# Optimization experiments

Hardware: AMD Instinct MI355X
Metric: run time of the kernel (lower is better)

The kernel has to match this reference:

```python
import math
import jax
import jax.numpy as jnp
import numpy as np

MUL = 32            # multiplicity of 0e and 1o in irreps_in/out
N_NODES = 50000
N_EDGES = 800000
N_BASIS = 10
N_HID = 100
NUM_NEIGHBORS = 16.0


def setup_inputs() -> dict:
    key = jax.random.key(0)
    ks = jax.random.split(key, 14)
    return {
        "node_input": jax.random.normal(ks[0], (N_NODES, 4 * MUL), jnp.float32),
        "node_attr": jnp.ones((N_NODES, 1), jnp.float32),
        "edge_src": jax.random.randint(ks[1], (N_EDGES,), 0, N_NODES, dtype=jnp.int32),
        "edge_dst": jax.random.randint(ks[2], (N_EDGES,), 0, N_NODES, dtype=jnp.int32),
        "edge_attr": jax.random.normal(ks[3], (N_EDGES, 4), jnp.float32),
        "edge_length_embedded": jax.random.uniform(ks[4], (N_EDGES, N_BASIS), dtype=jnp.float32),
        "W_sc0": jax.random.normal(ks[5], (MUL, MUL), jnp.float32),
        "W_sc1": jax.random.normal(ks[6], (MUL, MUL), jnp.float32),
        "W_l10": jax.random.normal(ks[7], (MUL, MUL), jnp.float32),
        "W_l11": jax.random.normal(ks[8], (MUL, MUL), jnp.float32),
        "W_l20": jax.random.normal(ks[9], (2 * MUL, MUL), jnp.float32),
        "W_l21": jax.random.normal(ks[10], (2 * MUL, MUL), jnp.float32),
        "W_fc1": jax.random.normal(ks[11], (N_BASIS, N_HID), jnp.float32),
        "W_fc2": jax.random.normal(ks[12], (N_HID, 4 * MUL), jnp.float32),
    }


def _fctp(x0, x1, attr, W0, W1):
    """FullyConnectedTensorProduct with a 1x0e attr: per-irrep linear * scalar attr.
    x0: [N,U], x1: [N,U,3], attr: [N,1]. Path norm alpha = 1/sqrt(fan_in)."""
    inv = 1.0 / math.sqrt(W0.shape[0])
    o0 = attr * (x0 @ W0) * inv                                    # [N,W]
    o1 = attr[:, :, None] * jnp.einsum("nud,uw->nwd", x1, W1) * inv  # [N,W,3]
    return o0, o1


def _forward(node_input, node_attr, edge_attr, edge_length_embedded,
             W_sc0, W_sc1, W_l10, W_l11, W_l20, W_l21, W_fc1, W_fc2,
             edge_src, edge_dst):
    N = node_input.shape[0]
    x0 = node_input[:, :MUL]                       # [N,32]  0e
    x1 = node_input[:, MUL:].reshape(N, MUL, 3)    # [N,32,3] 1o

    # self-connection and lin1 (both attr is scalar 0e)
    s0, s1 = _fctp(x0, x1, node_attr, W_sc0, W_sc1)
    y0, y1 = _fctp(x0, x1, node_attr, W_l10, W_l11)

    # radial MLP -> per-edge uvu weights (weight_numel = 4*MUL)
    h = jax.nn.silu(edge_length_embedded @ W_fc1 * (1.0 / math.sqrt(N_BASIS)))
    w = h @ W_fc2 * (1.0 / math.sqrt(N_HID))       # [E,128]
    w1, w2, w3, w4 = (w[:, 0*MUL:1*MUL], w[:, 1*MUL:2*MUL],
                      w[:, 2*MUL:3*MUL], w[:, 3*MUL:4*MUL])

    # gather source node features per edge
    x0s = y0[edge_src]                              # [E,32]
    x1s = y1[edge_src]                              # [E,32,3]
    ea0 = edge_attr[:, :1]                          # [E,1]   0e
    ea1 = edge_attr[:, 1:]                          # [E,3]   1o

    # segmented uvu tensor product (CG for lmax=1, component norm)
    mid0a = w1 * x0s * ea0                                         # 0e x 0e -> 0e
    mid0b = w4 * jnp.einsum("eum,em->eu", x1s, ea1) * (1.0 / math.sqrt(3.0))  # 1o x 1o -> 0e
    mid1a = (w2 * x0s)[:, :, None] * ea1[:, None, :]               # 0e x 1o -> 1o
    mid1b = w3[:, :, None] * x1s * ea0[:, None, :]                 # 1o x 0e -> 1o
    E = edge_attr.shape[0]
    edge_features = jnp.concatenate(
        [mid0a, mid0b, mid1a.reshape(E, -1), mid1b.reshape(E, -1)], axis=1)  # [E,256]

    # scatter-add to destination nodes
    agg = jax.ops.segment_sum(edge_features, edge_dst, num_segments=N)
    agg = agg * (1.0 / math.sqrt(NUM_NEIGHBORS))

    m0 = agg[:, :2 * MUL]                           # [N,64]  0e part of irreps_mid
    m1 = agg[:, 2 * MUL:].reshape(N, 2 * MUL, 3)    # [N,64,3] 1o part
    z0, z1 = _fctp(m0, m1, node_attr, W_l20, W_l21)

    # sc output_mask is all ones (every output irrep reachable)
    c_s = math.sin(math.pi / 8.0)
    c_x = math.cos(math.pi / 8.0)
    out0 = c_s * s0 + c_x * z0
    out1 = c_s * s1 + c_x * z1
    return jnp.concatenate([out0, out1.reshape(N, -1)], axis=1)   # [N,128]


def reference(node_input, node_attr, edge_src, edge_dst, edge_attr, edge_length_embedded,
              W_sc0, W_sc1, W_l10, W_l11, W_l20, W_l21, W_fc1, W_fc2):
    return _forward(node_input, node_attr, edge_attr, edge_length_embedded,
                    W_sc0, W_sc1, W_l10, W_l11, W_l20, W_l21, W_fc1, W_fc2,
                    edge_src, edge_dst)
```

## Files before the change

### kernel.cpp

```cpp
#include <hip/hip_runtime.h>
#include <hip/hip_bf16.h>

#define MUL 32
#define F4 128
#define NB 10
#define NH 100
#define EROW 136
#define REC 48

#define INV_SQRT32 0.17677669529663687f
#define INV_SQRT10 0.31622776601683794f
#define INV_SQRT100 0.1f
#define INV_SQRT3 0.5773502691896258f
#define AGG_SCALE 0.25f
#define INV8 0.125f
#define C_S 0.3826834323650898f
#define C_X 0.9238795325112867f

typedef __attribute__((ext_vector_type(8))) short short8;
typedef __attribute__((ext_vector_type(4))) float float4v;

__device__ __forceinline__ float bf2f(__hip_bfloat16 v) { return __bfloat162float(v); }
__device__ __forceinline__ unsigned short f2b(float x) {
    __hip_bfloat16 b = __float2bfloat16(x);
    return *(unsigned short*)&b;
}
__device__ __forceinline__ float b2f(unsigned short u) {
    __hip_bfloat16 b;
    *(unsigned short*)&b = u;
    return __bfloat162float(b);
}
__device__ __forceinline__ float ldin(const void* p, size_t i, int f) {
    return f ? ((const float*)p)[i] : bf2f(((const __hip_bfloat16*)p)[i]);
}

__global__ void detect_dtype_kernel(const void* __restrict__ node_attr, int* __restrict__ flag) {
    unsigned w = *(const unsigned*)node_attr;
    *flag = (w == 0x3F800000u) ? 1 : 0;
}

__global__ __launch_bounds__(256) void prep_kernel(
    const void* __restrict__ Wfc1,
    const void* __restrict__ Wfc2,
    const void* __restrict__ Wl20,
    const void* __restrict__ Wl21,
    const int* __restrict__ flagp,
    unsigned short* __restrict__ w1t,
    unsigned short* __restrict__ w2t,
    unsigned short* __restrict__ w20t,
    unsigned short* __restrict__ w21t)
{
    int f = *flagp;
    int gi = blockIdx.x * 256 + threadIdx.x;
    if (gi < 128 * 128) {
        int n = gi >> 7, k = gi & 127;
        w2t[gi] = (k < NH) ? f2b(ldin(Wfc2, (size_t)k * 128 + n, f)) : 0;
    }
    if (gi < 32 * 64) {
        int v = gi >> 6, u = gi & 63;
        w20t[gi] = f2b(ldin(Wl20, (size_t)u * 32 + v, f));
        w21t[gi] = f2b(ldin(Wl21, (size_t)u * 32 + v, f));
    }
    if (gi < 112 * 32) {
        int n = gi >> 5, k = gi & 31;
        w1t[gi] = (k < NB && n < NH) ? f2b(ldin(Wfc1, (size_t)k * NH + n, f)) : 0;
    }
}

__global__ __launch_bounds__(256) void hist_kernel(
    const int* __restrict__ edst, int* __restrict__ cnt, int E)
{
    int i = blockIdx.x * 256 + threadIdx.x;
    if (i < E) atomicAdd(&cnt[edst[i]], 1);
}

__global__ __launch_bounds__(1024) void scanA_kernel(
    int* __restrict__ cnt, int* __restrict__ bsum, int N)
{
    __shared__ int wsum[16];
    int t = threadIdx.x, lane = t & 63, wid = t >> 6;
    int i = blockIdx.x * 1024 + t;
    int v = (i < N) ? cnt[i] : 0;
    int x = v;
#pragma unroll
    for (int d = 1; d < 64; d <<= 1) { int yv = __shfl_up(x, d); if (lane >= d) x += yv; }
    if (lane == 63) wsum[wid] = x;
    __syncthreads();
    if (wid == 0 && lane < 16) {
        int s = wsum[lane];
#pragma unroll
        for (int d = 1; d < 16; d <<= 1) { int yv = __shfl_up(s, d); if (lane >= d) s += yv; }
        wsum[lane] = s;
    }
    __syncthreads();
    int pre = (wid > 0 ? wsum[wid - 1] : 0);
    if (i < N) cnt[i] = pre + x - v;
    if (t == 0) bsum[blockIdx.x] = wsum[15];
}

__global__ __launch_bounds__(64) void scanB_kernel(int* __restrict__ bsum, int nb)
{
    int t = threadIdx.x;
    int carry = 0;
    for (int c0 = 0; c0 < nb; c0 += 64) {
        int idx = c0 + t;
        int v = (idx < nb) ? bsum[idx] : 0;
        int x = v;
#pragma unroll
        for (int d = 1; d < 64; d <<= 1) { int yv = __shfl_up(x, d); if (t >= d) x += yv; }
        if (idx < nb) bsum[idx] = carry + x - v;
        carry += __shfl(x, 63);
    }
}

__global__ __launch_bounds__(1024) void scanC_kernel(
    int* __restrict__ cnt, const int* __restrict__ bsum, int N)
{
    int i = blockIdx.x * 1024 + threadIdx.x;
    if (i < N) cnt[i] += bsum[blockIdx.x];
}

__global__ __launch_bounds__(256) void scatter_build_kernel(
    const int* __restrict__ edst,
    const int* __restrict__ esrc,
    const void* __restrict__ eattr,
    const void* __restrict__ ele,
    const int* __restrict__ flagp,
    int* __restrict__ cnt,
    unsigned char* __restrict__ rec, int E)
{
    int i = blockIdx.x * 256 + threadIdx.x;
    if (i >= E) return;
    int f = *flagp;
    int d = edst[i];
    int p = atomicAdd(&cnt[d], 1);

    unsigned e0 = f2b(ldin(ele, (size_t)i * NB + 0, f));
    unsigned e1 = f2b(ldin(ele, (size_t)i * NB + 1, f));
    unsigned e2 = f2b(ldin(ele, (size_t)i * NB + 2, f));
    unsigned e3 = f2b(ldin(ele, (size_t)i * NB + 3, f));
    unsigned e4 = f2b(ldin(ele, (size_t)i * NB + 4, f));
    unsigned e5 = f2b(ldin(ele, (size_t)i * NB + 5, f));
    unsigned e6 = f2b(ldin(ele, (size_t)i * NB + 6, f));
    unsigned e7 = f2b(ldin(ele, (size_t)i * NB + 7, f));
    unsigned e8 = f2b(ldin(ele, (size_t)i * NB + 8, f));
    unsigned e9 = f2b(ldin(ele, (size_t)i * NB + 9, f));
    float ea0 = ldin(eattr, (size_t)i * 4 + 0, f);
    float ea1 = ldin(eattr, (size_t)i * 4 + 1, f);
    float ea2 = ldin(eattr, (size_t)i * 4 + 2, f);
    float ea3 = ldin(eattr, (size_t)i * 4 + 3, f);

    unsigned char* r = rec + (size_t)p * REC;
    *(int4*)(r + 0)  = make_int4(esrc[i], d, (int)(e0 | (e1 << 16)), (int)(e2 | (e3 << 16)));
    *(int4*)(r + 16) = make_int4((int)(e4 | (e5 << 16)), (int)(e6 | (e7 << 16)), (int)(e8 | (e9 << 16)), 0);
    *(float4*)(r + 32) = make_float4(ea0, ea1, ea2, ea3);
}

__global__ __launch_bounds__(256) void node_y_kernel(
    const void* __restrict__ node_input,
    const void* __restrict__ node_attr,
    const void* __restrict__ Wl10,
    const void* __restrict__ Wl11,
    const int* __restrict__ flagp,
    unsigned short* __restrict__ y, int N)
{
    __shared__ float sW0[1024];
    __shared__ float sW1[1024];
    __shared__ float sX[16 * 128];
    int f = *flagp;
    int t = threadIdx.x;
    for (int i = t; i < 1024; i += 256) {
        sW0[i] = ldin(Wl10, i, f);
        sW1[i] = ldin(Wl11, i, f);
    }
    int n0 = blockIdx.x * 16;
    for (int i = t; i < 2048; i += 256) {
        int ln = i >> 7, c = i & 127, n = n0 + ln;
        sX[i] = (n < N) ? ldin(node_input, (size_t)n * F4 + c, f) : 0.f;
    }
    __syncthreads();
    for (int i = t; i < 2048; i += 256) {
        int ln = i >> 7, c = i & 127, n = n0 + ln;
        if (n >= N) continue;
        float attr = ldin(node_attr, n, f);
        float acc = 0.f;
        if (c < 32) {
#pragma unroll
            for (int u = 0; u < 32; u++) acc += sX[ln * 128 + u] * sW0[u * 32 + c];
        } else {
            int d = (c - 32) >> 5, u0 = (c - 32) & 31;
#pragma unroll
            for (int u = 0; u < 32; u++) acc += sX[ln * 128 + 32 + u * 3 + d] * sW1[u * 32 + u0];
        }
        y[(size_t)n * F4 + c] = f2b(acc * attr * INV_SQRT32);
    }
}

#define SM_ELEB  0
#define SM_HW    4096
#define SM_EA    21504
#define SM_DST   22528
#define SM_TOTAL 22784

__global__ __launch_bounds__(256, 6) void fused_edge_kernel(
    const unsigned char* __restrict__ rec,
    const int* __restrict__ cnt,
    const unsigned short* __restrict__ y,
    const unsigned short* __restrict__ w1t,
    const unsigned short* __restrict__ w2t,
    const unsigned short* __restrict__ w20t,
    const unsigned short* __restrict__ w21t,
    float* __restrict__ agg,
    int E)
{
    __shared__ __align__(16) char smem[SM_TOTAL];
    unsigned short* sEleB = (unsigned short*)(smem + SM_ELEB);
    unsigned short* sHW = (unsigned short*)(smem + SM_HW);
    float* sEa = (float*)(smem + SM_EA);
    int* sDst = (int*)(smem + SM_DST);

    int t = threadIdx.x;
    int base = blockIdx.x * 64;
    int ne = E - base;
    if (ne > 64) ne = 64;

    int w = t >> 6, lane = t & 63;
    int lm = lane & 15, quad = lane >> 4;
    int em = w * 16 + lm;

    int src = (em < ne) ? *(const int*)(rec + (size_t)(base + em) * REC) : 0;
    const unsigned short* yrg = y + (size_t)src * 128;
    short8 x0  = *(const short8*)(yrg + quad * 8);
    short8 xd0 = *(const short8*)(yrg + 32 + quad * 8);
    short8 xd1 = *(const short8*)(yrg + 64 + quad * 8);
    short8 xd2 = *(const short8*)(yrg + 96 + quad * 8);

    if (t < 64)
        sDst[t] = (t < ne) ? *(const int*)(rec + (size_t)(base + t) * REC + 4) : -1;
    for (int i = t; i < 64 * 32; i += 256) {
        int e = i >> 5, k = i & 31;
        unsigned short v = 0;
        if (k < NB && e < ne)
            v = *(const unsigned short*)(rec + (size_t)(base + e) * REC + 8 + 2 * k);
        sEleB[i] = v;
    }
    {
        int e = t >> 2;
        sEa[t] = (e < ne) ? *(const float*)(rec + (size_t)(base + e) * REC + 32 + 4 * (t & 3)) : 0.f;
    }
    __syncthreads();

    {
        short8 a = *(const short8*)(sEleB + (w * 16 + lm) * 32 + quad * 8);
#pragma unroll
        for (int nt = 0; nt < 7; nt++) {
            float4v c1 = (float4v){0.f, 0.f, 0.f, 0.f};
            short8 b = *(const short8*)(w1t + (nt * 16 + lm) * 32 + quad * 8);
            c1 = __builtin_amdgcn_mfma_f32_16x16x32_bf16(a, b, c1, 0, 0, 0);
            int ch = nt * 16 + lm;
#pragma unroll
            for (int r = 0; r < 4; r++) {
                int row = w * 16 + quad * 4 + r;
                float hv = 0.f;
                if (ch < NH) {
                    float aa = c1[r] * INV_SQRT10;
                    hv = aa / (1.f + __expf(-aa));
                }
                sHW[row * EROW + ch] = f2b(hv);
            }
        }
        int e = t >> 2, seg = t & 3;
        *(uint2*)(sHW + e * EROW + 112 + seg * 4) = (uint2){0u, 0u};
    }
    __syncthreads();

    short8 hfr[4];
#pragma unroll
    for (int kc = 0; kc < 4; kc++)
        hfr[kc] = *(const short8*)(sHW + (w * 16 + lm) * EROW + kc * 32 + quad * 8);
    __syncthreads();
#pragma unroll
    for (int nt = 0; nt < 8; nt++) {
        float4v c2 = (float4v){0.f, 0.f, 0.f, 0.f};
#pragma unroll
        for (int kc = 0; kc < 4; kc++) {
            short8 b = *(const short8*)(w2t + (nt * 16 + lm) * 128 + kc * 32 + quad * 8);
            c2 = __builtin_amdgcn_mfma_f32_16x16x32_bf16(hfr[kc], b, c2, 0, 0, 0);
        }
#pragma unroll
        for (int r = 0; r < 4; r++)
            sHW[(w * 16 + quad * 4 + r) * EROW + nt * 16 + lm] = f2b(c2[r] * INV_SQRT100);
    }
    __syncthreads();

    {
        const unsigned short* wr = sHW + em * EROW;
        short8 wA = *(const short8*)(wr + quad * 8);
        short8 wB = *(const short8*)(wr + 32 + quad * 8);
        short8 wC = *(const short8*)(wr + 64 + quad * 8);
        short8 wD = *(const short8*)(wr + 96 + quad * 8);
        float ea0 = sEa[em * 4 + 0];
        float e1x = sEa[em * 4 + 1];
        float e1y = sEa[em * 4 + 2];
        float e1z = sEa[em * 4 + 3];
        float ea0S = ea0 * AGG_SCALE;
        float s3 = AGG_SCALE * INV_SQRT3;

        short8 f00, f01, f10, f11, f20, f21, f30, f31;
#pragma unroll
        for (int j = 0; j < 8; j++) {
            float x0f = b2f((unsigned short)x0[j]);
            float d0f = b2f((unsigned short)xd0[j]);
            float d1f = b2f((unsigned short)xd1[j]);
            float d2f = b2f((unsigned short)xd2[j]);
            f00[j] = (short)f2b(b2f((unsigned short)wA[j]) * x0f * ea0S);
            float tt = d0f * e1x + d1f * e1y + d2f * e1z;
            f01[j] = (short)f2b(b2f((unsigned short)wD[j]) * tt * s3);
            float p = b2f((unsigned short)wB[j]) * x0f * AGG_SCALE;
            f10[j] = (short)f2b(p * e1x);
            f20[j] = (short)f2b(p * e1y);
            f30[j] = (short)f2b(p * e1z);
            float q = b2f((unsigned short)wC[j]) * ea0S;
            f11[j] = (short)f2b(q * d0f);
            f21[j] = (short)f2b(q * d1f);
            f31[j] = (short)f2b(q * d2f);
        }

        __syncthreads();
        unsigned short* sFeat = (unsigned short*)smem;
#pragma unroll
        for (int g = 0; g < 4; g++) {
            const unsigned short* wt = g ? w21t : w20t;
            short8 ak0 = (g == 0) ? f00 : (g == 1) ? f10 : (g == 2) ? f20 : f30;
            short8 ak1 = (g == 0) ? f01 : (g == 1) ? f11 : (g == 2) ? f21 : f31;
#pragma unroll
            for (int nt = 0; nt < 2; nt++) {
                float4v acc = (float4v){0.f, 0.f, 0.f, 0.f};
                short8 b0 = *(const short8*)(wt + (nt * 16 + lm) * 64 + quad * 8);
                short8 b1 = *(const short8*)(wt + (nt * 16 + lm) * 64 + 32 + quad * 8);
                acc = __builtin_amdgcn_mfma_f32_16x16x32_bf16(ak0, b0, acc, 0, 0, 0);
                acc = __builtin_amdgcn_mfma_f32_16x16x32_bf16(ak1, b1, acc, 0, 0, 0);
                int ch = (g == 0) ? (nt * 16 + lm) : (32 + (g - 1) * 32 + nt * 16 + lm);
#pragma unroll
                for (int r = 0; r < 4; r++) {
                    int er = w * 16 + quad * 4 + r;
                    sFeat[er * EROW + ch] = f2b(acc[r]);
                }
            }
        }
        __syncthreads();

        if (t < 128) {
            int c = t;
            int e = 0;
            while (e < ne) {
                int d = sDst[e];
                int rs = e;
                do { e++; } while (e < ne && sDst[e] == d);
                if (d < 0) continue;
                float s = 0.f;
                for (int q = rs; q < e; q++) s += b2f(sFeat[q * EROW + c]);
                int bs = (d > 0) ? cnt[d - 1] : 0;
                int be = cnt[d];
                if (bs >= base && be <= base + ne)
                    agg[(size_t)d * F4 + c] = s;
                else
                    atomicAdd(&agg[(size_t)d * F4 + c], s);
            }
        }
    }
}

__global__ __launch_bounds__(256) void out_kernel(
    const void* __restrict__ node_input,
    const void* __restrict__ node_attr,
    const void* __restrict__ Wsc0,
    const void* __restrict__ Wsc1,
    const float* __restrict__ agg,
    const int* __restrict__ flagp,
    void* __restrict__ out, int N)
{
    __shared__ float sWs0[1024], sWs1[1024];
    __shared__ float sX[16 * 128];
    __shared__ float sA[16 * 128];
    int f = *flagp;
    int t = threadIdx.x;
    for (int i = t; i < 1024; i += 256) {
        sWs0[i] = ldin(Wsc0, i, f);
        sWs1[i] = ldin(Wsc1, i, f);
    }
    int n0 = blockIdx.x * 16;
    for (int i = t; i < 2048; i += 256) {
        int ln = i >> 7, c = i & 127, n = n0 + ln;
        sX[i] = (n < N) ? ldin(node_input, (size_t)n * F4 + c, f) : 0.f;
        sA[i] = (n < N) ? agg[(size_t)n * F4 + c] : 0.f;
    }
    __syncthreads();
    for (int i = t; i < 2048; i += 256) {
        int ln = i >> 7, c = i & 127, n = n0 + ln;
        if (n >= N) continue;
        float attr = ldin(node_attr, n, f);
        float s, z;
        if (c < 32) {
            float as = 0.f;
#pragma unroll
            for (int u = 0; u < 32; u++) as += sX[ln * 128 + u] * sWs0[u * 32 + c];
            s = as * INV_SQRT32;
            z = sA[ln * 128 + c];
        } else {
            int i2 = c - 32;
            int u0 = i2 / 3, d = i2 - u0 * 3;
            float as = 0.f;
#pragma unroll
            for (int u = 0; u < 32; u++) as += sX[ln * 128 + 32 + u * 3 + d] * sWs1[u * 32 + u0];
            s = as * INV_SQRT32;
            z = sA[ln * 128 + 32 + d * 32 + u0];
        }
        float val = attr * (C_S * s + C_X * z * INV8);
        size_t oi = (size_t)n * F4 + c;
        if (f) ((float*)out)[oi] = val;
        else   ((__hip_bfloat16*)out)[oi] = __float2bfloat16(val);
    }
}

extern "C" void kernel_launch(void* const* d_in, const int* in_sizes, int n_in,
                              void* d_out, int out_size, void* d_ws, size_t ws_size,
                              hipStream_t stream) {
    const void* node_input = d_in[0];
    const void* node_attr  = d_in[1];
    const int* edge_src    = (const int*)d_in[2];
    const int* edge_dst    = (const int*)d_in[3];
    const void* edge_attr  = d_in[4];
    const void* ele        = d_in[5];
    const void* Wsc0       = d_in[6];
    const void* Wsc1       = d_in[7];
    const void* Wl10       = d_in[8];
    const void* Wl11       = d_in[9];
    const void* Wl20       = d_in[10];
    const void* Wl21       = d_in[11];
    const void* Wfc1       = d_in[12];
    const void* Wfc2       = d_in[13];

    int N = in_sizes[0] / F4;
    int E = in_sizes[2];

    char* ws = (char*)d_ws;
    int* flag = (int*)ws;
    unsigned short* y = (unsigned short*)(ws + 64);
    size_t y_b = (size_t)N * F4 * 2;
    float* agg = (float*)(ws + 64 + y_b);
    size_t agg_b = (size_t)N * F4 * 4;
    size_t off = 64 + y_b + agg_b;
    unsigned short* w2t  = (unsigned short*)(ws + off);
    unsigned short* w20t = (unsigned short*)(ws + off + 32768);
    unsigned short* w21t = (unsigned short*)(ws + off + 36864);
    unsigned short* w1t  = (unsigned short*)(ws + off + 40960);
    size_t off2 = off + 49152;
    int* cnt = (int*)(ws + off2);
    size_t cnt_b = ((size_t)N * 4 + 63) & ~(size_t)63;
    int* bsum = (int*)(ws + off2 + cnt_b);
    size_t bsum_b = 4096;
    unsigned char* rec = (unsigned char*)(ws + off2 + cnt_b + bsum_b);

    int nscan = (N + 1023) / 1024;

    detect_dtype_kernel<<<1, 1, 0, stream>>>(node_attr, flag);
    prep_kernel<<<64, 256, 0, stream>>>(Wfc1, Wfc2, Wl20, Wl21, flag, w1t, w2t, w20t, w21t);
    (void)hipMemsetAsync(cnt, 0, (size_t)N * 4, stream);
    (void)hipMemsetAsync(agg, 0, agg_b, stream);

    hist_kernel<<<(E + 255) / 256, 256, 0, stream>>>(edge_dst, cnt, E);
    scanA_kernel<<<nscan, 1024, 0, stream>>>(cnt, bsum, N);
    scanB_kernel<<<1, 64, 0, stream>>>(bsum, nscan);
    scanC_kernel<<<nscan, 1024, 0, stream>>>(cnt, bsum, N);
    scatter_build_kernel<<<(E + 255) / 256, 256, 0, stream>>>(
        edge_dst, edge_src, edge_attr, ele, flag, cnt, rec, E);

    node_y_kernel<<<(N + 15) / 16, 256, 0, stream>>>(node_input, node_attr, Wl10, Wl11, flag, y, N);

    fused_edge_kernel<<<(E + 63) / 64, 256, 0, stream>>>(
        rec, cnt, y, w1t, w2t, w20t, w21t, agg, E);

    out_kernel<<<(N + 15) / 16, 256, 0, stream>>>(node_input, node_attr, Wsc0, Wsc1,
                                                  agg, flag, d_out, N);
}
```

Baseline: 611.1 us.

## Transpose feature tile and vectorize per-destination segmented reduction in edge kernel

Edge features are now stored channel-major in shared memory, so each reducing thread reads its channel's 64 edges with wide vector loads. Segment boundaries come from a wavefront ballot over the destination array, which replaces the serial while-loop and the global count lookups used to decide between a plain store and an atomic. Edge attributes are loaded straight into registers as a float4 instead of being staged in shared memory. The new rule stores non-atomically only when a segment is interior to the block, and it depends on edges being sorted by destination.

```diff
diff --git a/kernel.cpp b/kernel.cpp
--- a/kernel.cpp
+++ b/kernel.cpp
@@ -6,6 +6,7 @@
 #define NB 10
 #define NH 100
 #define EROW 136
+#define FROW 72
 #define REC 48
 
 #define INV_SQRT32 0.17677669529663687f
@@ -198,13 +199,11 @@
 
 #define SM_ELEB  0
 #define SM_HW    4096
-#define SM_EA    21504
-#define SM_DST   22528
-#define SM_TOTAL 22784
+#define SM_DST   21504
+#define SM_TOTAL 21760
 
 __global__ __launch_bounds__(256, 6) void fused_edge_kernel(
     const unsigned char* __restrict__ rec,
-    const int* __restrict__ cnt,
     const unsigned short* __restrict__ y,
     const unsigned short* __restrict__ w1t,
     const unsigned short* __restrict__ w2t,
@@ -216,7 +215,6 @@
     __shared__ __align__(16) char smem[SM_TOTAL];
     unsigned short* sEleB = (unsigned short*)(smem + SM_ELEB);
     unsigned short* sHW = (unsigned short*)(smem + SM_HW);
-    float* sEa = (float*)(smem + SM_EA);
     int* sDst = (int*)(smem + SM_DST);
 
     int t = threadIdx.x;
@@ -229,6 +227,8 @@
     int em = w * 16 + lm;
 
     int src = (em < ne) ? *(const int*)(rec + (size_t)(base + em) * REC) : 0;
+    float4 ea4 = (em < ne) ? *(const float4*)(rec + (size_t)(base + em) * REC + 32)
+                           : make_float4(0.f, 0.f, 0.f, 0.f);
     const unsigned short* yrg = y + (size_t)src * 128;
     short8 x0  = *(const short8*)(yrg + quad * 8);
     short8 xd0 = *(const short8*)(yrg + 32 + quad * 8);
@@ -243,10 +243,6 @@
         if (k < NB && e < ne)
             v = *(const unsigned short*)(rec + (size_t)(base + e) * REC + 8 + 2 * k);
         sEleB[i] = v;
-    }
-    {
-        int e = t >> 2;
-        sEa[t] = (e < ne) ? *(const float*)(rec + (size_t)(base + e) * REC + 32 + 4 * (t & 3)) : 0.f;
     }
     __syncthreads();
 
@@ -299,10 +295,10 @@
         short8 wB = *(const short8*)(wr + 32 + quad * 8);
         short8 wC = *(const short8*)(wr + 64 + quad * 8);
         short8 wD = *(const short8*)(wr + 96 + quad * 8);
-        float ea0 = sEa[em * 4 + 0];
-        float e1x = sEa[em * 4 + 1];
-        float e1y = sEa[em * 4 + 2];
-        float e1z = sEa[em * 4 + 3];
+        float ea0 = ea4.x;
+        float e1x = ea4.y;
+        float e1y = ea4.z;
+        float e1z = ea4.w;
         float ea0S = ea0 * AGG_SCALE;
         float s3 = AGG_SCALE * INV_SQRT3;
 
@@ -327,7 +323,7 @@
         }
 
         __syncthreads();
-        unsigned short* sFeat = (unsigned short*)smem;
+        unsigned short* sFeatT = (unsigned short*)smem;
 #pragma unroll
         for (int g = 0; g < 4; g++) {
             const unsigned short* wt = g ? w21t : w20t;
@@ -341,31 +337,40 @@
                 acc = __builtin_amdgcn_mfma_f32_16x16x32_bf16(ak0, b0, acc, 0, 0, 0);
                 acc = __builtin_amdgcn_mfma_f32_16x16x32_bf16(ak1, b1, acc, 0, 0, 0);
                 int ch = (g == 0) ? (nt * 16 + lm) : (32 + (g - 1) * 32 + nt * 16 + lm);
-#pragma unroll
-                for (int r = 0; r < 4; r++) {
-                    int er = w * 16 + quad * 4 + r;
-                    sFeat[er * EROW + ch] = f2b(acc[r]);
-                }
+                short4 sv;
+                sv.x = (short)f2b(acc[0]);
+                sv.y = (short)f2b(acc[1]);
+                sv.z = (short)f2b(acc[2]);
+                sv.w = (short)f2b(acc[3]);
+                *(short4*)(sFeatT + ch * FROW + (w * 16 + quad * 4)) = sv;
             }
         }
         __syncthreads();
 
         if (t < 128) {
             int c = t;
-            int e = 0;
-            while (e < ne) {
-                int d = sDst[e];
-                int rs = e;
-                do { e++; } while (e < ne && sDst[e] == d);
-                if (d < 0) continue;
-                float s = 0.f;
-                for (int q = rs; q < e; q++) s += b2f(sFeat[q * EROW + c]);
-                int bs = (d > 0) ? cnt[d - 1] : 0;
-                int be = cnt[d];
-                if (bs >= base && be <= base + ne)
-                    agg[(size_t)d * F4 + c] = s;
-                else
-                    atomicAdd(&agg[(size_t)d * F4 + c], s);
+            unsigned long long m =
+                __ballot((lane == 0) ? 1 : (sDst[lane] != sDst[lane - 1]));
+            const unsigned short* fr = sFeatT + c * FROW;
+            short8 fv[8];
+#pragma unroll
+            for (int q8 = 0; q8 < 8; q8++)
+                fv[q8] = *(const short8*)(fr + q8 * 8);
+            float s = 0.f;
+            int rs = 0;
+#pragma unroll
+            for (int e = 0; e < 64; e++) {
+                s += b2f((unsigned short)fv[e >> 3][e & 7]);
+                bool fl = (e == 63) || ((m >> (e + 1)) & 1ull);
+                if (fl) {
+                    int d = sDst[e];
+                    if (d >= 0) {
+                        if (rs > 0 && e < ne - 1) agg[(size_t)d * F4 + c] = s;
+                        else atomicAdd(&agg[(size_t)d * F4 + c], s);
+                    }
+                    s = 0.f;
+                    rs = e + 1;
+                }
             }
         }
     }
@@ -479,7 +484,7 @@
     node_y_kernel<<<(N + 15) / 16, 256, 0, stream>>>(node_input, node_attr, Wl10, Wl11, flag, y, N);
 
     fused_edge_kernel<<<(E + 63) / 64, 256, 0, stream>>>(
-        rec, cnt, y, w1t, w2t, w20t, w21t, agg, E);
+        rec, y, w1t, w2t, w20t, w21t, agg, E);
 
     out_kernel<<<(N + 15) / 16, 256, 0, stream>>>(node_input, node_attr, Wsc0, Wsc1,
                                                   agg, flag, d_out, N);
```

New measurement: 623.8 us. +2.1%, slower.
